# Kernel optimization log

Measured on AMD Instinct MI355X. Metric: run time of the kernel, lower is better.

Reference implementation:

```python
import jax, jax.numpy as jnp
import numpy as np

N, D, OUT, K = 1_000_000, 128, 128, 10
B2 = 4096            # final batch of nodes
B1 = B2 * K          # depth-1 frontier size


def setup_inputs() -> dict:
    key = jax.random.key(0)
    k1, k2, k3, k4, k5, k6, k7 = jax.random.split(key, 7)
    raw_features = jax.random.normal(k1, (N, D), dtype=jnp.float32)
    # SageLayer weights: [out, 2*in] (gcn=False => concat(self, agg))
    W1 = jax.random.normal(k2, (OUT, 2 * D), dtype=jnp.float32) * 0.05
    W2 = jax.random.normal(k3, (OUT, 2 * OUT), dtype=jnp.float32) * 0.05
    # depth-1 frontier node ids and their K sampled neighbors (global ids)
    nodes1 = jax.random.randint(k4, (B1,), 0, N)
    neigh1 = jax.random.randint(k5, (B1, K), 0, N)
    # batch nodes remapped to local indices into the depth-1 hidden table
    nodes2 = jax.random.randint(k6, (B2,), 0, B1)
    neigh2 = jax.random.randint(k7, (B2, K), 0, B1)
    return {"raw_features": raw_features, "W1": W1, "W2": W2,
            "nodes1": nodes1, "neigh1": neigh1,
            "nodes2": nodes2, "neigh2": neigh2}


def sage_layer(self_feats, agg_feats, W):
    # relu(concat(self, agg) @ W^T), matching SageLayer with gcn=False
    combined = jnp.concatenate([self_feats, agg_feats], axis=1)
    return jax.nn.relu(combined @ W.T)


def reference(raw_features, W1, W2, nodes1, neigh1, nodes2, neigh2):
    # Layer 1: mean-aggregate sampled neighbor raw features (gather + mean
    # replaces the dense mask.mm mean in the original).
    agg1 = jnp.mean(raw_features[neigh1], axis=1)      # [B1, D]
    h1 = sage_layer(raw_features[nodes1], agg1, W1)    # [B1, OUT]
    # Layer 2: neighbors indexed locally into the layer-1 hidden table
    agg2 = jnp.mean(h1[neigh2], axis=1)                # [B2, OUT]
    h2 = sage_layer(h1[nodes2], agg2, W2)              # [B2, OUT]
    return h2
```

## Files before the change

### kernel.cpp

```cpp
#include <hip/hip_runtime.h>


typedef __attribute__((ext_vector_type(8))) short  short8;
typedef __attribute__((ext_vector_type(8))) __bf16 bf16x8;
typedef __attribute__((ext_vector_type(4))) float  f32x4;

#define K_NEIGH 10
#define NB      32
#define PITCH   264

__device__ inline float b2f(short s) {
    union { unsigned int u; float f; } c;
    c.u = ((unsigned int)(unsigned short)s) << 16;
    return c.f;
}
__device__ inline short f2b(float f) {
    union { float f; unsigned int u; } c; c.f = f;
    unsigned int u = c.u;
    return (short)((u + 0x7fffu + ((u >> 16) & 1u)) >> 16);
}
__device__ inline bf16x8 as_bf16x8(short8 s) {
    union { short8 s; bf16x8 b; } c; c.s = s; return c.b;
}

__global__ void detect_f32(const unsigned short* __restrict__ w, int* __restrict__ flag) {
    if (threadIdx.x == 0 && blockIdx.x == 0) {
        int f = 0;
        for (int i = 0; i < 64; ++i) {
            unsigned int e = ((unsigned int)w[2 * i] >> 7) & 0xFFu;
            if (e >= 132u) f = 1;
        }
        *flag = f;
    }
}

__launch_bounds__(256, 4)
__global__ void gather_agg(const void* __restrict__ table,
                           const int*  __restrict__ nodes,
                           const int*  __restrict__ neigh,
                           short*      __restrict__ comb,
                           const int*  __restrict__ flag,
                           const int table_by_flag)
{
    const int idx  = blockIdx.x * 256 + threadIdx.x;
    const int node = idx >> 3;
    const int part = idx & 7;
    const bool t32 = table_by_flag && *flag;

    const int self_id = nodes[node];
    int nid[K_NEIGH];
#pragma unroll
    for (int k = 0; k < K_NEIGH; ++k) nid[k] = neigh[node * K_NEIGH + k];

    short8 s0, s1;
    float a[16];
#pragma unroll
    for (int i = 0; i < 16; ++i) a[i] = 0.f;

    if (!t32) {
        const short* base = (const short*)table;
        const short* srow = base + (long)self_id * 128 + part * 16;
        s0 = *(const short8*)(srow);
        s1 = *(const short8*)(srow + 8);
#pragma unroll
        for (int k = 0; k < K_NEIGH; ++k) {
            const short* nrow = base + (long)nid[k] * 128 + part * 16;
            short8 v0 = *(const short8*)(nrow);
            short8 v1 = *(const short8*)(nrow + 8);
#pragma unroll
            for (int i = 0; i < 8; ++i) { a[i] += b2f(v0[i]); a[8 + i] += b2f(v1[i]); }
        }
    } else {
        const float* base = (const float*)table;
        const float* srow = base + (long)self_id * 128 + part * 16;
        f32x4 u0 = *(const f32x4*)(srow);
        f32x4 u1 = *(const f32x4*)(srow + 4);
        f32x4 u2 = *(const f32x4*)(srow + 8);
        f32x4 u3 = *(const f32x4*)(srow + 12);
#pragma unroll
        for (int i = 0; i < 4; ++i) {
            s0[i] = f2b(u0[i]); s0[4 + i] = f2b(u1[i]);
            s1[i] = f2b(u2[i]); s1[4 + i] = f2b(u3[i]);
        }
#pragma unroll
        for (int k = 0; k < K_NEIGH; ++k) {
            const float* nrow = base + (long)nid[k] * 128 + part * 16;
            f32x4 v0 = *(const f32x4*)(nrow);
            f32x4 v1 = *(const f32x4*)(nrow + 4);
            f32x4 v2 = *(const f32x4*)(nrow + 8);
            f32x4 v3 = *(const f32x4*)(nrow + 12);
#pragma unroll
            for (int i = 0; i < 4; ++i) {
                a[i] += v0[i]; a[4 + i] += v1[i]; a[8 + i] += v2[i]; a[12 + i] += v3[i];
            }
        }
    }
    short8 g0, g1;
#pragma unroll
    for (int i = 0; i < 8; ++i) { g0[i] = f2b(a[i] * 0.1f); g1[i] = f2b(a[8 + i] * 0.1f); }
    short* dst = comb + (long)node * 256 + part * 16;
    *(short8*)(dst)       = s0;
    *(short8*)(dst + 8)   = s1;
    *(short8*)(dst + 128) = g0;
    *(short8*)(dst + 136) = g1;
}

__launch_bounds__(256, 2)
__global__ void gemm_combined(const short* __restrict__ comb,
                              const void* __restrict__ Wv,
                              void*       __restrict__ outv,
                              const int*  __restrict__ flag,
                              const int out_by_flag)
{
    __shared__ __align__(16) short lds[NB * PITCH];
    const int t    = threadIdx.x;
    const int blk  = blockIdx.x;
    const int lane = t & 63;
    const int wave = t >> 6;
    const int n15  = lane & 15;
    const int q    = lane >> 4;
    const int f32in = *flag;
    const bool o32 = out_by_flag && f32in;

    short8 bfrag[2][8];
    if (!f32in) {
        const short* W = (const short*)Wv;
#pragma unroll
        for (int ot = 0; ot < 2; ++ot) {
            const int o = wave * 32 + ot * 16 + n15;
#pragma unroll
            for (int fk = 0; fk < 8; ++fk)
                bfrag[ot][fk] = *(const short8*)(W + o * 256 + fk * 32 + q * 8);
        }
    } else {
        const float* W = (const float*)Wv;
#pragma unroll
        for (int ot = 0; ot < 2; ++ot) {
            const int o = wave * 32 + ot * 16 + n15;
#pragma unroll
            for (int fk = 0; fk < 8; ++fk) {
                const float* p = W + o * 256 + fk * 32 + q * 8;
                f32x4 v0 = *(const f32x4*)p;
                f32x4 v1 = *(const f32x4*)(p + 4);
                short8 s;
#pragma unroll
                for (int i = 0; i < 4; ++i) { s[i] = f2b(v0[i]); s[4 + i] = f2b(v1[i]); }
                bfrag[ot][fk] = s;
            }
        }
    }

    {
        const int m   = t >> 3;
        const int col = (t & 7) * 32;
        const short* src = comb + (long)blk * (NB * 256) + m * 256 + col;
        short8 x0 = *(const short8*)(src);
        short8 x1 = *(const short8*)(src + 8);
        short8 x2 = *(const short8*)(src + 16);
        short8 x3 = *(const short8*)(src + 24);
        short* dst = lds + m * PITCH + col;
        *(short8*)(dst)      = x0;
        *(short8*)(dst + 8)  = x1;
        *(short8*)(dst + 16) = x2;
        *(short8*)(dst + 24) = x3;
    }
    __syncthreads();

    f32x4 acc[2][2] = {};
#pragma unroll
    for (int mb = 0; mb < 2; ++mb) {
        const short* arow = lds + (mb * 16 + n15) * PITCH + q * 8;
        short8 af[8];
#pragma unroll
        for (int fk = 0; fk < 8; ++fk) af[fk] = *(const short8*)(arow + fk * 32);
#pragma unroll
        for (int ot = 0; ot < 2; ++ot)
#pragma unroll
            for (int fk = 0; fk < 8; ++fk)
                acc[mb][ot] = __builtin_amdgcn_mfma_f32_16x16x32_bf16(
                    as_bf16x8(af[fk]), as_bf16x8(bfrag[ot][fk]), acc[mb][ot], 0, 0, 0);
    }

#pragma unroll
    for (int mb = 0; mb < 2; ++mb)
#pragma unroll
        for (int ot = 0; ot < 2; ++ot) {
            const int col = wave * 32 + ot * 16 + n15;
#pragma unroll
            for (int r = 0; r < 4; ++r) {
                const long row = blk * NB + mb * 16 + q * 4 + r;
                float v = acc[mb][ot][r];
                v = v > 0.f ? v : 0.f;
                if (!o32) ((short*)outv)[row * 128 + col] = f2b(v);
                else      ((float*)outv)[row * 128 + col] = v;
            }
        }
}

__launch_bounds__(256, 2)
__global__ void sage_layer(const void* __restrict__ table,
                           const void* __restrict__ Wv,
                           const int*  __restrict__ nodes,
                           const int*  __restrict__ neigh,
                           void*       __restrict__ outv,
                           const int*  __restrict__ flag,
                           const int table_by_flag, const int out_by_flag)
{
    __shared__ __align__(16) short lds[NB * PITCH];
    const int t    = threadIdx.x;
    const int blk  = blockIdx.x;
    const int lane = t & 63;
    const int wave = t >> 6;
    const int n15  = lane & 15;
    const int q    = lane >> 4;
    const int f32in = *flag;
    const bool t32 = table_by_flag && f32in;
    const bool o32 = out_by_flag && f32in;

    short8 bfrag[2][8];
    if (!f32in) {
        const short* W = (const short*)Wv;
#pragma unroll
        for (int ot = 0; ot < 2; ++ot) {
            const int o = wave * 32 + ot * 16 + n15;
#pragma unroll
            for (int fk = 0; fk < 8; ++fk)
                bfrag[ot][fk] = *(const short8*)(W + o * 256 + fk * 32 + q * 8);
        }
    } else {
        const float* W = (const float*)Wv;
#pragma unroll
        for (int ot = 0; ot < 2; ++ot) {
            const int o = wave * 32 + ot * 16 + n15;
#pragma unroll
            for (int fk = 0; fk < 8; ++fk) {
                const float* p = W + o * 256 + fk * 32 + q * 8;
                f32x4 v0 = *(const f32x4*)p;
                f32x4 v1 = *(const f32x4*)(p + 4);
                short8 s;
#pragma unroll
                for (int i = 0; i < 4; ++i) { s[i] = f2b(v0[i]); s[4 + i] = f2b(v1[i]); }
                bfrag[ot][fk] = s;
            }
        }
    }

    {
        const int m    = t >> 3;
        const int part = t & 7;
        const int gi   = blk * NB + m;
        const int self_id = nodes[gi];
        int nidv[K_NEIGH];
#pragma unroll
        for (int k = 0; k < K_NEIGH; ++k) nidv[k] = neigh[gi * K_NEIGH + k];
        short8 s0, s1;
        float a[16];
#pragma unroll
        for (int i = 0; i < 16; ++i) a[i] = 0.f;

        if (!t32) {
            const short* srow = (const short*)table + (long)self_id * 128 + part * 16;
            s0 = *(const short8*)(srow);
            s1 = *(const short8*)(srow + 8);
#pragma unroll
            for (int k = 0; k < K_NEIGH; ++k) {
                const short* nrow = (const short*)table + (long)nidv[k] * 128 + part * 16;
                short8 v0 = *(const short8*)(nrow);
                short8 v1 = *(const short8*)(nrow + 8);
#pragma unroll
                for (int i = 0; i < 8; ++i) { a[i] += b2f(v0[i]); a[8 + i] += b2f(v1[i]); }
            }
        } else {
            const float* srow = (const float*)table + (long)self_id * 128 + part * 16;
            f32x4 u0 = *(const f32x4*)(srow);
            f32x4 u1 = *(const f32x4*)(srow + 4);
            f32x4 u2 = *(const f32x4*)(srow + 8);
            f32x4 u3 = *(const f32x4*)(srow + 12);
#pragma unroll
            for (int i = 0; i < 4; ++i) {
                s0[i] = f2b(u0[i]); s0[4 + i] = f2b(u1[i]);
                s1[i] = f2b(u2[i]); s1[4 + i] = f2b(u3[i]);
            }
#pragma unroll
            for (int k = 0; k < K_NEIGH; ++k) {
                const float* nrow = (const float*)table + (long)nidv[k] * 128 + part * 16;
                f32x4 v0 = *(const f32x4*)(nrow);
                f32x4 v1 = *(const f32x4*)(nrow + 4);
                f32x4 v2 = *(const f32x4*)(nrow + 8);
                f32x4 v3 = *(const f32x4*)(nrow + 12);
#pragma unroll
                for (int i = 0; i < 4; ++i) {
                    a[i] += v0[i]; a[4 + i] += v1[i]; a[8 + i] += v2[i]; a[12 + i] += v3[i];
                }
            }
        }
        short8 g0, g1;
#pragma unroll
        for (int i = 0; i < 8; ++i) { g0[i] = f2b(a[i] * 0.1f); g1[i] = f2b(a[8 + i] * 0.1f); }
        short* dst = lds + m * PITCH + part * 16;
        *(short8*)(dst)       = s0;
        *(short8*)(dst + 8)   = s1;
        *(short8*)(dst + 128) = g0;
        *(short8*)(dst + 136) = g1;
    }
    __syncthreads();

    f32x4 acc[2][2] = {};
#pragma unroll
    for (int mb = 0; mb < 2; ++mb) {
        const short* arow = lds + (mb * 16 + n15) * PITCH + q * 8;
        short8 af[8];
#pragma unroll
        for (int fk = 0; fk < 8; ++fk) af[fk] = *(const short8*)(arow + fk * 32);
#pragma unroll
        for (int ot = 0; ot < 2; ++ot)
#pragma unroll
            for (int fk = 0; fk < 8; ++fk)
                acc[mb][ot] = __builtin_amdgcn_mfma_f32_16x16x32_bf16(
                    as_bf16x8(af[fk]), as_bf16x8(bfrag[ot][fk]), acc[mb][ot], 0, 0, 0);
    }

#pragma unroll
    for (int mb = 0; mb < 2; ++mb)
#pragma unroll
        for (int ot = 0; ot < 2; ++ot) {
            const int col = wave * 32 + ot * 16 + n15;
#pragma unroll
            for (int r = 0; r < 4; ++r) {
                const long row = blk * NB + mb * 16 + q * 4 + r;
                float v = acc[mb][ot][r];
                v = v > 0.f ? v : 0.f;
                if (!o32) ((short*)outv)[row * 128 + col] = f2b(v);
                else      ((float*)outv)[row * 128 + col] = v;
            }
        }
}

extern "C" void kernel_launch(void* const* d_in, const int* in_sizes, int n_in,
                              void* d_out, int out_size, void* d_ws, size_t ws_size,
                              hipStream_t stream) {
    const void* raw    = d_in[0];
    const void* W1     = d_in[1];
    const void* W2     = d_in[2];
    const int*  nodes1 = (const int*)d_in[3];
    const int*  neigh1 = (const int*)d_in[4];
    const int*  nodes2 = (const int*)d_in[5];
    const int*  neigh2 = (const int*)d_in[6];

    int*   flag = (int*)d_ws;
    short* h1   = (short*)((char*)d_ws + 256);
    short* comb = (short*)((char*)d_ws + 256 + 10485760);

    const int B1 = in_sizes[3];
    const int B2 = in_sizes[5];

    detect_f32<<<1, 64, 0, stream>>>((const unsigned short*)W1, flag);
    gather_agg<<<(B1 * 8) / 256, 256, 0, stream>>>(raw, nodes1, neigh1, comb, flag,
                                                   1);
    gemm_combined<<<B1 / NB, 256, 0, stream>>>(comb, W1, h1, flag, 0);
    sage_layer<<<B2 / NB, 256, 0, stream>>>(h1, W2, nodes2, neigh2, d_out, flag,
                                            0, 1);
}
```

Measured before the change: 635.0 us.

## Map one wavefront per node in gather kernel and parallelize dtype detection

The layer-1 gather/mean kernel now assigns a whole 64-lane wavefront to each node, with each lane handling two features, instead of 8 threads per node each handling 16 features. All ten neighbor rows are loaded up front so many loads are in flight, and the occupancy hint is raised. The dtype detection kernel uses a wavefront ballot instead of a serial loop on one thread. The aim is coalesced row reads and more memory-level parallelism for the random gathers, at the cost of narrower per-lane loads and redundant index loads across lanes.

Measured after the change: 630.8 us. No clear change (-0.7%).

```diff
diff --git a/kernel.cpp b/kernel.cpp
--- a/kernel.cpp
+++ b/kernel.cpp
@@ -19,22 +19,22 @@
     unsigned int u = c.u;
     return (short)((u + 0x7fffu + ((u >> 16) & 1u)) >> 16);
 }
+__device__ inline unsigned int pack2(float lo, float hi) {
+    return (unsigned int)(unsigned short)f2b(lo)
+         | ((unsigned int)(unsigned short)f2b(hi) << 16);
+}
 __device__ inline bf16x8 as_bf16x8(short8 s) {
     union { short8 s; bf16x8 b; } c; c.s = s; return c.b;
 }
 
 __global__ void detect_f32(const unsigned short* __restrict__ w, int* __restrict__ flag) {
-    if (threadIdx.x == 0 && blockIdx.x == 0) {
-        int f = 0;
-        for (int i = 0; i < 64; ++i) {
-            unsigned int e = ((unsigned int)w[2 * i] >> 7) & 0xFFu;
-            if (e >= 132u) f = 1;
-        }
-        *flag = f;
-    }
-}
-
-__launch_bounds__(256, 4)
+    const int lane = threadIdx.x;
+    unsigned int e = ((unsigned int)w[2 * lane] >> 7) & 0xFFu;
+    unsigned long long m = __ballot(e >= 132u);
+    if (lane == 0) *flag = (m != 0ull) ? 1 : 0;
+}
+
+__launch_bounds__(256, 8)
 __global__ void gather_agg(const void* __restrict__ table,
                            const int*  __restrict__ nodes,
                            const int*  __restrict__ neigh,
@@ -42,9 +42,9 @@
                            const int*  __restrict__ flag,
                            const int table_by_flag)
 {
-    const int idx  = blockIdx.x * 256 + threadIdx.x;
-    const int node = idx >> 3;
-    const int part = idx & 7;
+    const int t    = threadIdx.x;
+    const int lane = t & 63;
+    const int node = blockIdx.x * 4 + (t >> 6);
     const bool t32 = table_by_flag && *flag;
 
     const int self_id = nodes[node];
@@ -52,57 +52,36 @@
 #pragma unroll
     for (int k = 0; k < K_NEIGH; ++k) nid[k] = neigh[node * K_NEIGH + k];
 
-    short8 s0, s1;
-    float a[16];
-#pragma unroll
-    for (int i = 0; i < 16; ++i) a[i] = 0.f;
-
-    if (!t32) {
+    unsigned int sp;
+    float a0 = 0.f, a1 = 0.f;
+
+    if (t32) {
+        const float* base = (const float*)table;
+        float2 self = *(const float2*)(base + (long)self_id * 128 + lane * 2);
+        float2 v[K_NEIGH];
+#pragma unroll
+        for (int k = 0; k < K_NEIGH; ++k)
+            v[k] = *(const float2*)(base + (long)nid[k] * 128 + lane * 2);
+#pragma unroll
+        for (int k = 0; k < K_NEIGH; ++k) { a0 += v[k].x; a1 += v[k].y; }
+        sp = pack2(self.x, self.y);
+    } else {
         const short* base = (const short*)table;
-        const short* srow = base + (long)self_id * 128 + part * 16;
-        s0 = *(const short8*)(srow);
-        s1 = *(const short8*)(srow + 8);
+        sp = *(const unsigned int*)(base + (long)self_id * 128 + lane * 2);
+        unsigned int v[K_NEIGH];
+#pragma unroll
+        for (int k = 0; k < K_NEIGH; ++k)
+            v[k] = *(const unsigned int*)(base + (long)nid[k] * 128 + lane * 2);
 #pragma unroll
         for (int k = 0; k < K_NEIGH; ++k) {
-            const short* nrow = base + (long)nid[k] * 128 + part * 16;
-            short8 v0 = *(const short8*)(nrow);
-            short8 v1 = *(const short8*)(nrow + 8);
-#pragma unroll
-            for (int i = 0; i < 8; ++i) { a[i] += b2f(v0[i]); a[8 + i] += b2f(v1[i]); }
-        }
-    } else {
-        const float* base = (const float*)table;
-        const float* srow = base + (long)self_id * 128 + part * 16;
-        f32x4 u0 = *(const f32x4*)(srow);
-        f32x4 u1 = *(const f32x4*)(srow + 4);
-        f32x4 u2 = *(const f32x4*)(srow + 8);
-        f32x4 u3 = *(const f32x4*)(srow + 12);
-#pragma unroll
-        for (int i = 0; i < 4; ++i) {
-            s0[i] = f2b(u0[i]); s0[4 + i] = f2b(u1[i]);
-            s1[i] = f2b(u2[i]); s1[4 + i] = f2b(u3[i]);
-        }
-#pragma unroll
-        for (int k = 0; k < K_NEIGH; ++k) {
-            const float* nrow = base + (long)nid[k] * 128 + part * 16;
-            f32x4 v0 = *(const f32x4*)(nrow);
-            f32x4 v1 = *(const f32x4*)(nrow + 4);
-            f32x4 v2 = *(const f32x4*)(nrow + 8);
-            f32x4 v3 = *(const f32x4*)(nrow + 12);
-#pragma unroll
-            for (int i = 0; i < 4; ++i) {
-                a[i] += v0[i]; a[4 + i] += v1[i]; a[8 + i] += v2[i]; a[12 + i] += v3[i];
-            }
-        }
-    }
-    short8 g0, g1;
-#pragma unroll
-    for (int i = 0; i < 8; ++i) { g0[i] = f2b(a[i] * 0.1f); g1[i] = f2b(a[8 + i] * 0.1f); }
-    short* dst = comb + (long)node * 256 + part * 16;
-    *(short8*)(dst)       = s0;
-    *(short8*)(dst + 8)   = s1;
-    *(short8*)(dst + 128) = g0;
-    *(short8*)(dst + 136) = g1;
+            a0 += b2f((short)(v[k] & 0xFFFFu));
+            a1 += b2f((short)(v[k] >> 16));
+        }
+    }
+    unsigned int gp = pack2(a0 * 0.1f, a1 * 0.1f);
+    unsigned int* crow = (unsigned int*)(comb + (long)node * 256);
+    crow[lane]      = sp;
+    crow[64 + lane] = gp;
 }
 
 __launch_bounds__(256, 2)
@@ -355,8 +334,8 @@
     const int B2 = in_sizes[5];
 
     detect_f32<<<1, 64, 0, stream>>>((const unsigned short*)W1, flag);
-    gather_agg<<<(B1 * 8) / 256, 256, 0, stream>>>(raw, nodes1, neigh1, comb, flag,
-                                                   1);
+    gather_agg<<<B1 / 4, 256, 0, stream>>>(raw, nodes1, neigh1, comb, flag,
+                                           1);
     gemm_combined<<<B1 / NB, 256, 0, stream>>>(comb, W1, h1, flag, 0);
     sage_layer<<<B2 / NB, 256, 0, stream>>>(h1, W2, nodes2, neigh2, d_out, flag,
                                             0, 1);
```
